# Kernel optimization log

Measured on AMD Instinct MI355X. Metric: run time of the kernel, lower is better.

## Reference

```python
import jax, jax.numpy as jnp
import numpy as np

L, H, N, F, E, FF, OUT, B = 4, 8, 1024, 128, 128, 512, 64, 32


def setup_inputs() -> dict:
    key = jax.random.key(0)
    ks = jax.random.split(key, 16)
    s = 0.02
    return {
        "x": jax.random.normal(ks[0], (B, N, F), jnp.float32),
        "adj": jax.random.randint(ks[1], (N, N), 0, 2, jnp.int32),
        "Ws": jax.random.normal(ks[2], (L, H, E, F), jnp.float32) * s,
        "bs": jnp.zeros((L, H, E), jnp.float32),
        "As": jax.random.normal(ks[3], (L, H, 2 * E, N), jnp.float32) * s,
        "W1": jax.random.normal(ks[4], (L, FF, F), jnp.float32) * s,
        "b1": jnp.zeros((L, FF), jnp.float32),
        "W2": jax.random.normal(ks[5], (L, F, FF), jnp.float32) * s,
        "b2": jnp.zeros((L, F), jnp.float32),
        "g1": jnp.ones((L, F), jnp.float32),
        "be1": jnp.zeros((L, F), jnp.float32),
        "g2": jnp.ones((L, F), jnp.float32),
        "be2": jnp.zeros((L, F), jnp.float32),
        "Wo": jax.random.normal(ks[6], (OUT, N * F), jnp.float32) * s,
        "bo": jnp.zeros((OUT,), jnp.float32),
    }


def _ln(x, g, b, eps=1e-5):
    m = jnp.mean(x, axis=-1, keepdims=True)
    v = jnp.mean((x - m) ** 2, axis=-1, keepdims=True)
    return (x - m) / jnp.sqrt(v + eps) * g + b


def reference(x, adj, Ws, bs, As, W1, b1, W2, b2, g1, be1, g2, be2, Wo, bo):
    # mask[j, i] = 1 if j is a neighbor of i (adj_matrix[:, i] > 0 in torch source)
    mask = (adj > 0).astype(x.dtype)
    E_ = Ws.shape[2]
    for l in range(Ws.shape[0]):
        # per-head projection: h [B, H, N, E]
        h = jnp.einsum('bnf,hef->bhne', x, Ws[l]) + bs[l][None, :, None, :]
        # score[b,h,i] = h_i . a[:E, i] + (sum_{j in N(i)} h_j) . a[E:, i]
        s1 = jnp.einsum('bhne,hen->bhn', h, As[l][:, :E_, :])
        hn = jnp.einsum('jn,bhje->bhne', mask, h)  # neighbor sums
        s2 = jnp.einsum('bhne,hen->bhn', hn, As[l][:, E_:, :])
        score = s1 + s2  # [B, H, N]
        # attention row i is the constant score[b,h,i] broadcast over columns,
        # so attention @ h == score[...,None] * h.sum(over nodes)
        hsum = h.sum(axis=2)  # [B, H, E]
        hp = score[..., None] * hsum[:, :, None, :]  # [B, H, N, E]
        att = jax.nn.leaky_relu(hp, 0.01).sum(axis=1)  # sum over heads -> [B, N, F]
        x = _ln(x + att, g1[l], be1[l])
        ff = jax.nn.relu(x @ W1[l].T + b1[l]) @ W2[l].T + b2[l]
        x = _ln(x + ff, g2[l], be2[l])
    flat = x.reshape(x.shape[0], -1)  # [B, N*F]
    return jax.nn.relu(flat) @ Wo.T + bo
```

## Files before the change

kernel.cpp:

```cpp
#include <hip/hip_runtime.h>

#define L_ 4
#define H_ 8
#define Nn 1024
#define F_ 128
#define E_ 128
#define FF_ 512
#define OUT_ 64
#define B_ 32
#define KTOT (Nn * F_)

typedef unsigned short u16;
typedef __bf16 bf16_t;
typedef __attribute__((ext_vector_type(8))) __bf16 bf16x8;
typedef __attribute__((ext_vector_type(4))) float f32x4;

__device__ __forceinline__ u16 f2b(float v) {
    bf16_t h = (bf16_t)v;
    return __builtin_bit_cast(u16, h);
}
__device__ __forceinline__ float b2f(u16 u) {
    unsigned v = (unsigned)u << 16;
    return __builtin_bit_cast(float, v);
}

typedef const __attribute__((address_space(1))) void* gvp;
typedef __attribute__((address_space(3))) void* lvp;
__device__ __forceinline__ void gll16(const void* g, void* l) {
    __builtin_amdgcn_global_load_lds((gvp)g, (lvp)l, 16, 0, 0);
}

template <int R>
__device__ __forceinline__ void stage(const u16* __restrict__ g, int ldg,
                                      u16* lds, int w, int l) {
    const int r8 = l >> 3, jq = l & 7;
#pragma unroll
    for (int i = 0; i < R / 32; ++i) {
        const int row0 = w * (R / 4) + i * 8;
        const int row = row0 + r8;
        gll16(g + (long)row * ldg + ((jq ^ (row & 7)) << 3), lds + row0 * 64);
    }
}

__device__ __forceinline__ void stage128x64(const u16* __restrict__ g, int ldg,
                                            u16* lds, int w, int l) {
    const int r8 = l >> 3, jq = l & 7;
#pragma unroll
    for (int i = 0; i < 2; ++i) {
        const int row0 = i * 64 + w * 8;
        const int row = row0 + r8;
        gll16(g + (long)row * ldg + ((jq ^ (row & 7)) << 3), lds + row0 * 64);
    }
}

template <int BM, int BN, bool DUAL, int EPI, int BSH, bool GSWAP, bool DBUF>
__global__ __launch_bounds__(256) void k_mfma(
    const u16* __restrict__ A, int lda, long sAz,
    const u16* __restrict__ Bhp, const u16* __restrict__ Blp, int ldb, long sBz,
    const float* __restrict__ bias,
    float* __restrict__ Cf, u16* __restrict__ Cb, int ldc, long sCz, int K)
{
    constexpr int WN = (BN == 64) ? 1 : ((BM == 64) ? 4 : 2);
    constexpr int WM = 4 / WN;
    constexpr int SM = BM / WM, SN = BN / WN;
    constexpr int MF = SM / 16, NF = SN / 16;
    constexpr int BUFE = BM * 64 + (DUAL ? 2 : 1) * BN * 64;
    __shared__ __align__(16) u16 lds[BUFE * (DBUF ? 2 : 1)];
    const int t = threadIdx.x;
    const int w = t >> 6, l = t & 63, lr = l & 15, lg = l >> 4;
    const int wm0 = (w / WN) * SM, wn0 = (w % WN) * SN;
    const int bidm = GSWAP ? blockIdx.z : blockIdx.x;
    const int bidz = GSWAP ? blockIdx.x : blockIdx.z;
    const int m0 = bidm * BM, n0 = blockIdx.y * BN;
    A += BSH ? ((long)(bidz >> 1) * sAz + (long)(bidz & 1) * 128)
             : (long)bidz * sAz;
    Bhp += (long)(bidz >> BSH) * sBz;
    if (DUAL) Blp += (long)bidz * sBz;

    f32x4 acc[MF][NF] = {};

    auto stageAll = [&](u16* base, int k0) {
        stage<BM>(A + (long)m0 * lda + k0, lda, base, w, l);
        stage<BN>(Bhp + (long)n0 * ldb + k0, ldb, base + BM * 64, w, l);
        if (DUAL) stage<BN>(Blp + (long)n0 * ldb + k0, ldb, base + BM * 64 + BN * 64, w, l);
    };
    auto compute = [&](const u16* base) {
        const u16* Al = base;
        const u16* Bh = base + BM * 64;
        const u16* Bl = Bh + BN * 64;
#pragma unroll
        for (int ks = 0; ks < 2; ++ks) {
            bf16x8 af[MF], bh[NF], bl[NF];
            const int kq = ks * 4 + lg;
#pragma unroll
            for (int mf = 0; mf < MF; ++mf) {
                int row = wm0 + mf * 16 + lr;
                af[mf] = *reinterpret_cast<const bf16x8*>(&Al[row * 64 + ((kq ^ (row & 7)) << 3)]);
            }
#pragma unroll
            for (int nf = 0; nf < NF; ++nf) {
                int row = wn0 + nf * 16 + lr;
                int off = row * 64 + ((kq ^ (row & 7)) << 3);
                bh[nf] = *reinterpret_cast<const bf16x8*>(&Bh[off]);
                if (DUAL) bl[nf] = *reinterpret_cast<const bf16x8*>(&Bl[off]);
            }
#pragma unroll
            for (int mf = 0; mf < MF; ++mf)
#pragma unroll
                for (int nf = 0; nf < NF; ++nf) {
                    acc[mf][nf] = __builtin_amdgcn_mfma_f32_16x16x32_bf16(af[mf], bh[nf], acc[mf][nf], 0, 0, 0);
                    if (DUAL)
                        acc[mf][nf] = __builtin_amdgcn_mfma_f32_16x16x32_bf16(af[mf], bl[nf], acc[mf][nf], 0, 0, 0);
                }
        }
    };

    if (DBUF) {
        stageAll(lds, 0);
        __syncthreads();
        int cur = 0;
        for (int k0 = 0; k0 < K; k0 += 64) {
            if (k0 + 64 < K) stageAll(lds + (cur ^ 1) * BUFE, k0 + 64);
            compute(lds + cur * BUFE);
            __syncthreads();
            cur ^= 1;
        }
    } else {
        for (int k0 = 0; k0 < K; k0 += 64) {
            __syncthreads();
            stageAll(lds, k0);
            __syncthreads();
            compute(lds);
        }
    }

    float bv[NF];
    if (EPI == 1) {
#pragma unroll
        for (int nf = 0; nf < NF; ++nf) bv[nf] = bias[n0 + wn0 + nf * 16 + lr];
    }
    if (EPI == 1 || EPI == 3) Cb += (long)bidz * sCz;
    else                      Cf += (long)bidz * sCz;
#pragma unroll
    for (int mf = 0; mf < MF; ++mf)
#pragma unroll
        for (int nf = 0; nf < NF; ++nf)
#pragma unroll
            for (int r = 0; r < 4; ++r) {
                long row = m0 + wm0 + mf * 16 + lg * 4 + r;
                int col = n0 + wn0 + nf * 16 + lr;
                float v = acc[mf][nf][r];
                if (EPI == 1) Cb[row * ldc + col] = f2b(fmaxf(v + bv[nf], 0.f));
                else if (EPI == 3) Cb[row * ldc + col] = f2b(v);
                else Cf[row * ldc + col] = v;
            }
}

template <bool LAST>
__global__ __launch_bounds__(512) void k_ff_ln2(
    const u16* __restrict__ xb,
    const u16* __restrict__ W1b,
    const float* __restrict__ b1,
    const u16* __restrict__ W2b,
    const float* __restrict__ b2,
    float* __restrict__ xc,
    const float* __restrict__ g, const float* __restrict__ be,
    u16* __restrict__ xh,
    float* __restrict__ xsp,
    u16* __restrict__ xrb)
{
    __shared__ __align__(16) u16 lds[65536];
    const int t = threadIdx.x;
    const int w = t >> 6, l = t & 63, lr = l & 15, lg = l >> 4;
    const int wr = w >> 2, wc = w & 3;
    const int wn0 = wc * 32;
    const int m0 = blockIdx.x * 128;
    u16* A0 = lds;
    u16* P0 = lds + 16384;
    u16* Wb0 = lds + 32768;
    u16* Wb1 = lds + 49152;

    stage128x64(xb + (long)m0 * F_,      F_, A0, w, l);
    stage128x64(xb + (long)m0 * F_ + 64, F_, A0 + 8192, w, l);
    stage128x64(W1b,      F_, Wb0, w, l);
    stage128x64(W1b + 64, F_, Wb0 + 8192, w, l);
    float xcr[32];
#pragma unroll
    for (int rr = 0; rr < 16; ++rr) {
        const long xof = (long)(m0 + w * 16 + rr) * F_;
        xcr[rr * 2]     = xc[xof + l];
        xcr[rr * 2 + 1] = xc[xof + l + 64];
    }
    __syncthreads();

    f32x4 acc2[4][2] = {};
    for (int c = 0; c < 4; ++c) {
        stage128x64(W2b + c * 128,      FF_, Wb1, w, l);
        stage128x64(W2b + c * 128 + 64, FF_, Wb1 + 8192, w, l);
        f32x4 acc1[4][2] = {};
#pragma unroll
        for (int s = 0; s < 4; ++s) {
            const int kh = s >> 1, kq = (s & 1) * 4 + lg;
            bf16x8 af[4], bfr[2];
#pragma unroll
            for (int mf = 0; mf < 4; ++mf) {
                int row = wr * 64 + mf * 16 + lr;
                af[mf] = *reinterpret_cast<const bf16x8*>(
                    &A0[kh * 8192 + row * 64 + ((kq ^ (row & 7)) << 3)]);
            }
#pragma unroll
            for (int nf = 0; nf < 2; ++nf) {
                int row = wn0 + nf * 16 + lr;
                bfr[nf] = *reinterpret_cast<const bf16x8*>(
                    &Wb0[kh * 8192 + row * 64 + ((kq ^ (row & 7)) << 3)]);
            }
#pragma unroll
            for (int mf = 0; mf < 4; ++mf)
#pragma unroll
                for (int nf = 0; nf < 2; ++nf)
                    acc1[mf][nf] = __builtin_amdgcn_mfma_f32_16x16x32_bf16(af[mf], bfr[nf], acc1[mf][nf], 0, 0, 0);
        }
        float b1v[2] = { b1[c * 128 + wn0 + lr], b1[c * 128 + wn0 + 16 + lr] };
#pragma unroll
        for (int mf = 0; mf < 4; ++mf)
#pragma unroll
            for (int nf = 0; nf < 2; ++nf)
#pragma unroll
                for (int r = 0; r < 4; ++r) {
                    int row = wr * 64 + mf * 16 + lg * 4 + r;
                    int sp = (row ^ (row >> 3)) & 7;
                    int cc = wn0 + nf * 16 + lr;
                    int c6 = cc & 63;
                    float v = fmaxf(acc1[mf][nf][r] + b1v[nf], 0.f);
                    P0[(cc >> 6) * 8192 + row * 64 + (((c6 >> 3) ^ sp) << 3) + (c6 & 7)] = f2b(v);
                }
        __syncthreads();
        if (c < 3) {
            stage128x64(W1b + (long)(c + 1) * 128 * F_,      F_, Wb0, w, l);
            stage128x64(W1b + (long)(c + 1) * 128 * F_ + 64, F_, Wb0 + 8192, w, l);
        }
#pragma unroll
        for (int s = 0; s < 4; ++s) {
            const int kh = s >> 1, kq = (s & 1) * 4 + lg;
            bf16x8 af[4], bfr[2];
#pragma unroll
            for (int mf = 0; mf < 4; ++mf) {
                int row = wr * 64 + mf * 16 + lr;
                int sp = (row ^ (row >> 3)) & 7;
                af[mf] = *reinterpret_cast<const bf16x8*>(
                    &P0[kh * 8192 + row * 64 + ((kq ^ sp) << 3)]);
            }
#pragma unroll
            for (int nf = 0; nf < 2; ++nf) {
                int row = wn0 + nf * 16 + lr;
                bfr[nf] = *reinterpret_cast<const bf16x8*>(
                    &Wb1[kh * 8192 + row * 64 + ((kq ^ (row & 7)) << 3)]);
            }
#pragma unroll
            for (int mf = 0; mf < 4; ++mf)
#pragma unroll
                for (int nf = 0; nf < 2; ++nf)
                    acc2[mf][nf] = __builtin_amdgcn_mfma_f32_16x16x32_bf16(af[mf], bfr[nf], acc2[mf][nf], 0, 0, 0);
        }
        __syncthreads();
    }
    float (*buf)[132] = (float(*)[132])lds;
    float (*ps)[128]  = (float(*)[128])((char*)lds + 69632);
    float bv[2] = { b2[wn0 + lr], b2[wn0 + 16 + lr] };
#pragma unroll
    for (int mf = 0; mf < 4; ++mf)
#pragma unroll
        for (int nf = 0; nf < 2; ++nf)
#pragma unroll
            for (int r = 0; r < 4; ++r)
                buf[wr * 64 + mf * 16 + lg * 4 + r][wn0 + nf * 16 + lr] = acc2[mf][nf][r] + bv[nf];
    __syncthreads();
    const float gl0 = g[l], gl1 = g[l + 64], bl0 = be[l], bl1 = be[l + 64];
    float s0 = 0.f, s1 = 0.f;
#pragma unroll
    for (int rr = 0; rr < 16; ++rr) {
        const int row = w * 16 + rr;
        const long xb_ = (long)(m0 + row) * F_;
        float v0 = buf[row][l] + xcr[rr * 2];
        float v1 = buf[row][l + 64] + xcr[rr * 2 + 1];
        float sum = v0 + v1;
#pragma unroll
        for (int o = 32; o; o >>= 1) sum += __shfl_xor(sum, o);
        const float mean = sum * (1.f / 128.f);
        const float d0 = v0 - mean, d1 = v1 - mean;
        float vs = d0 * d0 + d1 * d1;
#pragma unroll
        for (int o = 32; o; o >>= 1) vs += __shfl_xor(vs, o);
        const float rstd = rsqrtf(vs * (1.f / 128.f) + 1e-5f);
        float o0 = d0 * rstd * gl0 + bl0;
        float o1 = d1 * rstd * gl1 + bl1;
        if (LAST) {
            xrb[xb_ + l] = f2b(fmaxf(o0, 0.f));
            xrb[xb_ + l + 64] = f2b(fmaxf(o1, 0.f));
        } else {
            xc[xb_ + l] = o0;       xc[xb_ + l + 64] = o1;
            buf[row][l] = o0;       buf[row][l + 64] = o1;
            s0 += o0;               s1 += o1;
        }
    }
    if (!LAST) {
        ps[w][l] = s0; ps[w][l + 64] = s1;
        __syncthreads();
        const int b = m0 >> 10, nb0 = m0 & 1023, seg = (m0 >> 7) & 7;
        const int n8 = (t & 15) * 8, fb = t >> 4;
#pragma unroll
        for (int i = 0; i < 4; ++i) {
            const int f = fb + 32 * i;
            union { u16 u[8]; float4 v; } Hv;
#pragma unroll
            for (int j = 0; j < 8; ++j) Hv.u[j] = f2b(buf[n8 + j][f]);
            *reinterpret_cast<float4*>(&xh[((long)b * F_ + f) * Nn + nb0 + n8]) = Hv.v;
        }
        if (t < 128) {
            float s = 0.f;
#pragma unroll
            for (int k = 0; k < 8; ++k) s += ps[k][t];
            xsp[((long)b * 8 + seg) * 128 + t] = s;
        }
    }
}

__global__ __launch_bounds__(256) void k_final_mfma(
    const u16* __restrict__ xrb, const u16* __restrict__ Wob,
    float* __restrict__ part)
{
    __shared__ __align__(16) u16 Al[32 * 512];
    const int c = blockIdx.x;
    const long k0 = (long)c * 512;
    const int t = threadIdx.x, w = t >> 6, l = t & 63, lr = l & 15, lg = l >> 4;
#pragma unroll
    for (int i = 0; i < 8; ++i) {
        int ch = i * 256 + t, row = ch >> 6, jq = ch & 63;
        *reinterpret_cast<float4*>(&Al[row * 512 + ((jq ^ (row & 7)) << 3)]) =
            *reinterpret_cast<const float4*>(&xrb[(long)row * KTOT + k0 + (jq << 3)]);
    }
    __syncthreads();
    f32x4 acc[2] = {};
    const u16* Bp = Wob + (long)(w * 16 + lr) * KTOT + k0 + lg * 8;
#pragma unroll
    for (int ks = 0; ks < 16; ++ks) {
        bf16x8 bfr = *reinterpret_cast<const bf16x8*>(Bp + ks * 32);
        const int j8 = ks * 4 + lg;
#pragma unroll
        for (int mf = 0; mf < 2; ++mf) {
            int row = mf * 16 + lr;
            bf16x8 af = *reinterpret_cast<const bf16x8*>(&Al[row * 512 + ((j8 ^ (row & 7)) << 3)]);
            acc[mf] = __builtin_amdgcn_mfma_f32_16x16x32_bf16(af, bfr, acc[mf], 0, 0, 0);
        }
    }
#pragma unroll
    for (int mf = 0; mf < 2; ++mf)
#pragma unroll
        for (int r = 0; r < 4; ++r) {
            int b = mf * 16 + lg * 4 + r, o = w * 16 + lr;
            part[((long)c * B_ + b) * OUT_ + o] = acc[mf][r];
        }
}

__global__ void k_final_reduce(const float* __restrict__ part,
                               const float* __restrict__ bo, float* __restrict__ out)
{
    int i = blockIdx.x * 256 + threadIdx.x;
    int o = i & 63;
    float s = bo[o];
    for (int c = 0; c < 256; ++c) s += part[(long)c * (B_ * OUT_) + i];
    out[i] = s;
}

__global__ __launch_bounds__(256) void k_maskT(const int* __restrict__ adj,
                                               u16* __restrict__ maskTb,
                                               int* __restrict__ degi)
{
    __shared__ u16 tl[64][65];
    const int j0 = blockIdx.x * 64, n0 = blockIdx.y * 64, t = threadIdx.x;
#pragma unroll
    for (int i = 0; i < 16; ++i) {
        int s = i * 256 + t, jl = s >> 6, nl = s & 63;
        tl[jl][nl] = (adj[(long)(j0 + jl) * Nn + n0 + nl] > 0) ? 0x3F80 : 0;
    }
    __syncthreads();
    if (t < 64) {
        int c = 0;
#pragma unroll
        for (int jl = 0; jl < 64; ++jl) c += (tl[jl][t] != 0);
        atomicAdd(&degi[n0 + t], c);
    }
#pragma unroll
    for (int i = 0; i < 16; ++i) {
        int s = i * 256 + t, nl = s >> 6, jl = s & 63;
        maskTb[(long)(n0 + nl) * Nn + j0 + jl] = tl[jl][nl];
    }
}

__global__ __launch_bounds__(256) void k_tpb(const float* __restrict__ in,
                                             u16* __restrict__ out, int R, int C)
{
    __shared__ float tl[64][65];
    const int c0 = blockIdx.x * 64, r0 = blockIdx.y * 64, t = threadIdx.x;
    in  += (long)blockIdx.z * R * C;
    out += (long)blockIdx.z * R * C;
#pragma unroll
    for (int i = 0; i < 16; ++i) {
        int s = i * 256 + t, rl = s >> 6, cl = s & 63;
        tl[rl][cl] = in[(long)(r0 + rl) * C + c0 + cl];
    }
    __syncthreads();
#pragma unroll
    for (int i = 0; i < 16; ++i) {
        int s = i * 256 + t, cl = s >> 6, rl = s & 63;
        out[(long)(c0 + cl) * R + r0 + rl] = f2b(tl[rl][cl]);
    }
}

__global__ void k_cvtW(const float* __restrict__ W1, const float* __restrict__ W2,
                       u16* __restrict__ W1b, u16* __restrict__ W2b)
{
    int i = blockIdx.x * 256 + threadIdx.x;
    W1b[i] = f2b(W1[i]);
    W2b[i] = f2b(W2[i]);
}

__global__ void k_cvtWo(const float* __restrict__ Wo, u16* __restrict__ Wob)
{
    long i = ((long)blockIdx.x * 256 + threadIdx.x) * 8;
    float4 a = *reinterpret_cast<const float4*>(&Wo[i]);
    float4 b = *reinterpret_cast<const float4*>(&Wo[i + 4]);
    union { u16 u[8]; float4 v; } r;
    r.u[0] = f2b(a.x); r.u[1] = f2b(a.y); r.u[2] = f2b(a.z); r.u[3] = f2b(a.w);
    r.u[4] = f2b(b.x); r.u[5] = f2b(b.y); r.u[6] = f2b(b.z); r.u[7] = f2b(b.w);
    *reinterpret_cast<float4*>(&Wob[i]) = r.v;
}

__global__ __launch_bounds__(256) void k_xpose(const float* __restrict__ x,
                                               u16* __restrict__ xh)
{
    __shared__ float tile[64][132];
    const int b = blockIdx.y, n0 = blockIdx.x * 64, t = threadIdx.x;
#pragma unroll
    for (int i = 0; i < 8; ++i) {
        int s = i * 256 + t, nl = s >> 5, f4 = (s & 31) << 2;
        float4 v = *reinterpret_cast<const float4*>(&x[((long)b * Nn + n0 + nl) * F_ + f4]);
        tile[nl][f4] = v.x; tile[nl][f4 + 1] = v.y;
        tile[nl][f4 + 2] = v.z; tile[nl][f4 + 3] = v.w;
    }
    __syncthreads();
    const int f = t >> 1, nb = (t & 1) << 5;
    const long ob = ((long)b * F_ + f) * Nn + n0 + nb;
    union { u16 u[8]; float4 v; } Hv;
#pragma unroll
    for (int i = 0; i < 32; i += 8) {
#pragma unroll
        for (int j = 0; j < 8; ++j) Hv.u[j] = f2b(tile[nb + i + j][f]);
        *reinterpret_cast<float4*>(&xh[ob + i]) = Hv.v;
    }
}

__global__ __launch_bounds__(256) void k_xs2(const float* __restrict__ x, float* __restrict__ xsp)
{
    __shared__ float sh[2][128];
    const int seg = blockIdx.x, b = blockIdx.y, t = threadIdx.x;
    const int f = t & 127, h2 = t >> 7;
    const float* p = x + ((long)b * Nn + seg * 128 + h2 * 64) * F_ + f;
    float s = 0.f;
    for (int i = 0; i < 64; ++i) s += p[(long)i * F_];
    sh[h2][f] = s;
    __syncthreads();
    if (t < 128) xsp[((long)b * 8 + seg) * 128 + t] = sh[0][t] + sh[1][t];
}

__global__ void k_hsum(const float* __restrict__ xsp, const float* __restrict__ Wl,
                       const float* __restrict__ bsl, float* __restrict__ hsum)
{
    __shared__ float xs[128];
    const int i = blockIdx.x * 256 + threadIdx.x;
    const int b = i >> 10;
    if (threadIdx.x < 128) {
        const float* xp = xsp + (long)b * 8 * 128 + threadIdx.x;
        float v = 0.f;
#pragma unroll
        for (int sg = 0; sg < 8; ++sg) v += xp[sg * 128];
        xs[threadIdx.x] = v;
    }
    __syncthreads();
    const int e = i & 127, h = (i >> 7) & 7;
    const float* w = Wl + ((long)h * E_ + e) * F_;
    float s = 0.f;
    for (int f = 0; f < F_; ++f) s += xs[f] * w[f];
    hsum[i] = s + (float)Nn * bsl[h * E_ + e];
}

__global__ void k_d12(const float* __restrict__ As, const float* __restrict__ bs,
                      float* __restrict__ d12all)
{
    const int lyr = blockIdx.y;
    const float* Asl = As + (long)lyr * H_ * 2 * E_ * Nn;
    const float* bsl = bs + (long)lyr * H_ * E_;
    int i = blockIdx.x * 256 + threadIdx.x;
    int n = i & 1023, h = (i >> 10) & 7, w = i >> 13;
    const float* a = Asl + ((long)h * 2 * E_ + (long)w * E_) * Nn + n;
    const float* bb = bsl + h * E_;
    float s = 0.f;
    for (int e = 0; e < E_; ++e) s += bb[e] * a[(long)e * Nn];
    d12all[(long)lyr * 2 * H_ * Nn + ((long)w * H_ + h) * Nn + n] = s;
}

__global__ __launch_bounds__(256) void k_score_ln1(
    float* __restrict__ x, const u16* __restrict__ y,
    const float* __restrict__ Ct, const float* __restrict__ d12,
    const int* __restrict__ degi, const float* __restrict__ hsum,
    const float* __restrict__ g, const float* __restrict__ be,
    u16* __restrict__ xb)
{
    const int n = blockIdx.x, t = threadIdx.x;
    __shared__ float c1[H_][128], c2[H_][128];
    __shared__ float sbs[H_];
#pragma unroll
    for (int i = 0; i < 4; ++i) {
        int s = i * 256 + t, h = s >> 7, f = s & 127;
        c1[h][f] = Ct[((long)(2 * h) * Nn + n) * F_ + f];
        c2[h][f] = Ct[((long)(2 * h + 1) * Nn + n) * F_ + f];
    }
    if (t < H_) sbs[t] = d12[(long)t * Nn + n] + (float)degi[n] * d12[(long)(H_ + t) * Nn + n];
    __syncthreads();
    const int w = t >> 6, l = t & 63;
    const float gl0 = g[l], gl1 = g[l + 64], bl0 = be[l], bl1 = be[l + 64];
    for (int bi = 0; bi < 8; ++bi) {
        const int b = w * 8 + bi;
        const long base = ((long)b * Nn + n) * F_;
        float x0 = x[base + l], x1 = x[base + l + 64];
        float y0 = b2f(y[base + l]), y1 = b2f(y[base + l + 64]);
        float a0 = 0.f, a1 = 0.f;
#pragma unroll
        for (int h = 0; h < H_; ++h) {
            float p = x0 * c1[h][l] + x1 * c1[h][l + 64]
                    + y0 * c2[h][l] + y1 * c2[h][l + 64];
#pragma unroll
            for (int o = 32; o; o >>= 1) p += __shfl_xor(p, o);
            float s = p + sbs[h];
            float h0 = hsum[((long)b * H_ + h) * E_ + l];
            float h1 = hsum[((long)b * H_ + h) * E_ + l + 64];
            float p0 = s * h0, p1 = s * h1;
            a0 += (p0 > 0.f ? p0 : 0.01f * p0);
            a1 += (p1 > 0.f ? p1 : 0.01f * p1);
        }
        float v0 = x0 + a0, v1 = x1 + a1;
        float sum = v0 + v1;
#pragma unroll
        for (int o = 32; o; o >>= 1) sum += __shfl_xor(sum, o);
        const float mean = sum * (1.f / 128.f);
        const float d0 = v0 - mean, d1 = v1 - mean;
        float vs = d0 * d0 + d1 * d1;
#pragma unroll
        for (int o = 32; o; o >>= 1) vs += __shfl_xor(vs, o);
        const float rstd = rsqrtf(vs * (1.f / 128.f) + 1e-5f);
        float o0 = d0 * rstd * gl0 + bl0;
        float o1 = d1 * rstd * gl1 + bl1;
        x[base + l] = o0;        x[base + l + 64] = o1;
        xb[base + l] = f2b(o0);  xb[base + l + 64] = f2b(o1);
    }
}

extern "C" void kernel_launch(void* const* d_in, const int* in_sizes, int n_in,
                              void* d_out, int out_size, void* d_ws, size_t ws_size,
                              hipStream_t stream)
{
    const float* x_in = (const float*)d_in[0];
    const int*   adj  = (const int*)d_in[1];
    const float* Ws   = (const float*)d_in[2];
    const float* bs   = (const float*)d_in[3];
    const float* As   = (const float*)d_in[4];
    const float* W1   = (const float*)d_in[5];
    const float* b1   = (const float*)d_in[6];
    const float* W2   = (const float*)d_in[7];
    const float* b2   = (const float*)d_in[8];
    const float* g1   = (const float*)d_in[9];
    const float* be1  = (const float*)d_in[10];
    const float* g2   = (const float*)d_in[11];
    const float* be2  = (const float*)d_in[12];
    const float* Wo   = (const float*)d_in[13];
    const float* bo   = (const float*)d_in[14];
    float* out = (float*)d_out;

    char* wsb = (char*)d_ws;
    u16*   maskTb = (u16*)wsb;
    float* xc     = (float*)(wsb + (2L << 20));
    u16*   yb     = (u16*)(wsb + (18L << 20));
    float* CtAll  = (float*)(wsb + (66L << 20));
    u16*   xb     = (u16*)(wsb + (98L << 20));
    u16*   xrb    = (u16*)(wsb + (106L << 20));
    u16*   Wob    = (u16*)(wsb + (114L << 20));
    float* part   = (float*)(wsb + (130L << 20));
    u16*   xTh    = (u16*)(wsb + (132L << 20));
    u16*   AsTb   = (u16*)(wsb + (148L << 20));
    u16*   WsTb   = (u16*)(wsb + (164L << 20));
    char*  S      = wsb + (166L << 20);
    int*   degi   = (int*)S;
    float* xsp    = (float*)(S + (4L << 10));
    float* hsum   = (float*)(S + (132L << 10));
    float* d12all = (float*)(S + (260L << 10));
    u16*   W1b    = (u16*)(S + (516L << 10));
    u16*   W2b    = (u16*)(S + (1028L << 10));

    hipMemsetAsync(degi, 0, Nn * sizeof(int), stream);
    hipMemcpyAsync(xc, x_in, sizeof(float) * (long)B_ * Nn * F_,
                   hipMemcpyDeviceToDevice, stream);
    k_maskT<<<dim3(16, 16), 256, 0, stream>>>(adj, maskTb, degi);
    k_cvtW<<<(L_ * FF_ * F_) / 256, 256, 0, stream>>>(W1, W2, W1b, W2b);
    k_cvtWo<<<(OUT_ * KTOT) / (256 * 8), 256, 0, stream>>>(Wo, Wob);
    k_tpb<<<dim3(16, 4, L_ * H_), 256, 0, stream>>>(As, AsTb, 2 * E_, Nn);
    k_tpb<<<dim3(2, 2, L_ * H_), 256, 0, stream>>>(Ws, WsTb, E_, F_);
    k_xpose<<<dim3(16, B_), 256, 0, stream>>>(x_in, xTh);
    k_xs2<<<dim3(8, B_), 256, 0, stream>>>(x_in, xsp);
    k_d12<<<dim3((2 * H_ * Nn) / 256, L_), 256, 0, stream>>>(As, bs, d12all);
    k_mfma<64, 128, false, 0, 1, false, false><<<dim3(16, 1, 64), 256, 0, stream>>>(
        AsTb, 2 * E_, (long)Nn * 2 * E_, WsTb, nullptr, E_, (long)F_ * E_,
        nullptr, CtAll, nullptr, F_, (long)Nn * F_, E_);

    for (int l = 0; l < L_; ++l) {
        const float* Wl  = Ws + (long)l * H_ * E_ * F_;
        const float* bsl = bs + (long)l * H_ * E_;

        k_mfma<128, 64, false, 3, 0, true, true><<<dim3(32, 2, 8), 256, 0, stream>>>(
            maskTb, Nn, 0L, xTh, nullptr, Nn, (long)F_ * Nn,
            nullptr, nullptr, yb, F_, (long)Nn * F_, Nn);

        k_hsum<<<(B_ * H_ * E_) / 256, 256, 0, stream>>>(xsp, Wl, bsl, hsum);
        k_score_ln1<<<Nn, 256, 0, stream>>>(
            xc, yb, CtAll + (long)l * 16 * Nn * F_, d12all + (long)l * 2 * H_ * Nn,
            degi, hsum, g1 + l * F_, be1 + l * F_, xb);
        if (l < L_ - 1)
            k_ff_ln2<false><<<256, 512, 0, stream>>>(
                xb, W1b + (long)l * FF_ * F_, b1 + l * FF_,
                W2b + (long)l * F_ * FF_, b2 + l * F_, xc,
                g2 + l * F_, be2 + l * F_, xTh, xsp, nullptr);
        else
            k_ff_ln2<true><<<256, 512, 0, stream>>>(
                xb, W1b + (long)l * FF_ * F_, b1 + l * FF_,
                W2b + (long)l * F_ * FF_, b2 + l * F_, xc,
                g2 + l * F_, be2 + l * F_, nullptr, nullptr, xrb);
    }

    k_final_mfma<<<256, 256, 0, stream>>>(xrb, Wob, part);
    k_final_reduce<<<(B_ * OUT_) / 256, 256, 0, stream>>>(part, bo, out);
}
```

Before: 372.7 us.

## Keep residual stream and Ct projection in bf16 to cut memory traffic

Replaces the fp32 residual buffer xc with bf16 ping-pong buffers (xA/xB). The LN2 residual is now read from the already staged bf16 tile in LDS instead of reloaded from global memory, and the output buffer moves to a non-overlapping LDS region. The precomputed Ct projection is also stored in bf16, and the initial fp32 device copy is replaced by a bf16 conversion kernel. This halves global reads and writes of the activations in score_ln1 and ff_ln2, at the cost of bf16 rounding in the residual path.

```diff
diff --git a/kernel.cpp b/kernel.cpp
--- a/kernel.cpp
+++ b/kernel.cpp
@@ -163,8 +163,8 @@
     const float* __restrict__ b1,
     const u16* __restrict__ W2b,
     const float* __restrict__ b2,
-    float* __restrict__ xc,
     const float* __restrict__ g, const float* __restrict__ be,
+    u16* __restrict__ xbn,
     u16* __restrict__ xh,
     float* __restrict__ xsp,
     u16* __restrict__ xrb)
@@ -184,13 +184,6 @@
     stage128x64(xb + (long)m0 * F_ + 64, F_, A0 + 8192, w, l);
     stage128x64(W1b,      F_, Wb0, w, l);
     stage128x64(W1b + 64, F_, Wb0 + 8192, w, l);
-    float xcr[32];
-#pragma unroll
-    for (int rr = 0; rr < 16; ++rr) {
-        const long xof = (long)(m0 + w * 16 + rr) * F_;
-        xcr[rr * 2]     = xc[xof + l];
-        xcr[rr * 2 + 1] = xc[xof + l + 64];
-    }
     __syncthreads();
 
     f32x4 acc2[4][2] = {};
@@ -264,8 +257,8 @@
         }
         __syncthreads();
     }
-    float (*buf)[132] = (float(*)[132])lds;
-    float (*ps)[128]  = (float(*)[128])((char*)lds + 69632);
+    float (*buf)[132] = (float(*)[132])((char*)lds + 32768);
+    float (*ps)[128]  = (float(*)[128])((char*)lds + 100352);
     float bv[2] = { b2[wn0 + lr], b2[wn0 + 16 + lr] };
 #pragma unroll
     for (int mf = 0; mf < 4; ++mf)
@@ -281,8 +274,11 @@
     for (int rr = 0; rr < 16; ++rr) {
         const int row = w * 16 + rr;
         const long xb_ = (long)(m0 + row) * F_;
-        float v0 = buf[row][l] + xcr[rr * 2];
-        float v1 = buf[row][l + 64] + xcr[rr * 2 + 1];
+        const int sw = (row & 7);
+        float r0 = b2f(A0[row * 64 + ((((l >> 3) ^ sw)) << 3) + (l & 7)]);
+        float r1 = b2f(A0[8192 + row * 64 + ((((l >> 3) ^ sw)) << 3) + (l & 7)]);
+        float v0 = buf[row][l] + r0;
+        float v1 = buf[row][l + 64] + r1;
         float sum = v0 + v1;
 #pragma unroll
         for (int o = 32; o; o >>= 1) sum += __shfl_xor(sum, o);
@@ -298,7 +294,8 @@
             xrb[xb_ + l] = f2b(fmaxf(o0, 0.f));
             xrb[xb_ + l + 64] = f2b(fmaxf(o1, 0.f));
         } else {
-            xc[xb_ + l] = o0;       xc[xb_ + l + 64] = o1;
+            xbn[xb_ + l] = f2b(o0);
+            xbn[xb_ + l + 64] = f2b(o1);
             buf[row][l] = o0;       buf[row][l + 64] = o1;
             s0 += o0;               s1 += o1;
         }
@@ -434,6 +431,17 @@
     r.u[0] = f2b(a.x); r.u[1] = f2b(a.y); r.u[2] = f2b(a.z); r.u[3] = f2b(a.w);
     r.u[4] = f2b(b.x); r.u[5] = f2b(b.y); r.u[6] = f2b(b.z); r.u[7] = f2b(b.w);
     *reinterpret_cast<float4*>(&Wob[i]) = r.v;
+}
+
+__global__ void k_cvtX(const float* __restrict__ x, u16* __restrict__ xo)
+{
+    long i = ((long)blockIdx.x * 256 + threadIdx.x) * 8;
+    float4 a = *reinterpret_cast<const float4*>(&x[i]);
+    float4 b = *reinterpret_cast<const float4*>(&x[i + 4]);
+    union { u16 u[8]; float4 v; } r;
+    r.u[0] = f2b(a.x); r.u[1] = f2b(a.y); r.u[2] = f2b(a.z); r.u[3] = f2b(a.w);
+    r.u[4] = f2b(b.x); r.u[5] = f2b(b.y); r.u[6] = f2b(b.z); r.u[7] = f2b(b.w);
+    *reinterpret_cast<float4*>(&xo[i]) = r.v;
 }
 
 __global__ __launch_bounds__(256) void k_xpose(const float* __restrict__ x,
@@ -510,8 +518,8 @@
 }
 
 __global__ __launch_bounds__(256) void k_score_ln1(
-    float* __restrict__ x, const u16* __restrict__ y,
-    const float* __restrict__ Ct, const float* __restrict__ d12,
+    const u16* __restrict__ xA, const u16* __restrict__ y,
+    const u16* __restrict__ Ctb, const float* __restrict__ d12,
     const int* __restrict__ degi, const float* __restrict__ hsum,
     const float* __restrict__ g, const float* __restrict__ be,
     u16* __restrict__ xb)
@@ -522,8 +530,8 @@
 #pragma unroll
     for (int i = 0; i < 4; ++i) {
         int s = i * 256 + t, h = s >> 7, f = s & 127;
-        c1[h][f] = Ct[((long)(2 * h) * Nn + n) * F_ + f];
-        c2[h][f] = Ct[((long)(2 * h + 1) * Nn + n) * F_ + f];
+        c1[h][f] = b2f(Ctb[((long)(2 * h) * Nn + n) * F_ + f]);
+        c2[h][f] = b2f(Ctb[((long)(2 * h + 1) * Nn + n) * F_ + f]);
     }
     if (t < H_) sbs[t] = d12[(long)t * Nn + n] + (float)degi[n] * d12[(long)(H_ + t) * Nn + n];
     __syncthreads();
@@ -532,8 +540,8 @@
     for (int bi = 0; bi < 8; ++bi) {
         const int b = w * 8 + bi;
         const long base = ((long)b * Nn + n) * F_;
-        float x0 = x[base + l], x1 = x[base + l + 64];
-        float y0 = b2f(y[base + l]), y1 = b2f(y[base + l + 64]);
+        float x0 = b2f(xA[base + l]), x1 = b2f(xA[base + l + 64]);
+        float y0 = b2f(y[base + l]),  y1 = b2f(y[base + l + 64]);
         float a0 = 0.f, a1 = 0.f;
 #pragma unroll
         for (int h = 0; h < H_; ++h) {
@@ -558,10 +566,8 @@
 #pragma unroll
         for (int o = 32; o; o >>= 1) vs += __shfl_xor(vs, o);
         const float rstd = rsqrtf(vs * (1.f / 128.f) + 1e-5f);
-        float o0 = d0 * rstd * gl0 + bl0;
-        float o1 = d1 * rstd * gl1 + bl1;
-        x[base + l] = o0;        x[base + l + 64] = o1;
-        xb[base + l] = f2b(o0);  xb[base + l + 64] = f2b(o1);
+        xb[base + l]      = f2b(d0 * rstd * gl0 + bl0);
+        xb[base + l + 64] = f2b(d1 * rstd * gl1 + bl1);
     }
 }
 
@@ -588,17 +594,17 @@
 
     char* wsb = (char*)d_ws;
     u16*   maskTb = (u16*)wsb;
-    float* xc     = (float*)(wsb + (2L << 20));
-    u16*   yb     = (u16*)(wsb + (18L << 20));
-    float* CtAll  = (float*)(wsb + (66L << 20));
-    u16*   xb     = (u16*)(wsb + (98L << 20));
-    u16*   xrb    = (u16*)(wsb + (106L << 20));
-    u16*   Wob    = (u16*)(wsb + (114L << 20));
-    float* part   = (float*)(wsb + (130L << 20));
-    u16*   xTh    = (u16*)(wsb + (132L << 20));
-    u16*   AsTb   = (u16*)(wsb + (148L << 20));
-    u16*   WsTb   = (u16*)(wsb + (164L << 20));
-    char*  S      = wsb + (166L << 20);
+    u16*   xA     = (u16*)(wsb + (2L << 20));
+    u16*   yb     = (u16*)(wsb + (10L << 20));
+    u16*   CtAllb = (u16*)(wsb + (18L << 20));
+    u16*   xB     = (u16*)(wsb + (34L << 20));
+    u16*   xrb    = (u16*)(wsb + (42L << 20));
+    u16*   Wob    = (u16*)(wsb + (50L << 20));
+    float* part   = (float*)(wsb + (66L << 20));
+    u16*   xTh    = (u16*)(wsb + (68L << 20));
+    u16*   AsTb   = (u16*)(wsb + (76L << 20));
+    u16*   WsTb   = (u16*)(wsb + (92L << 20));
+    char*  S      = wsb + (94L << 20);
     int*   degi   = (int*)S;
     float* xsp    = (float*)(S + (4L << 10));
     float* hsum   = (float*)(S + (132L << 10));
@@ -607,19 +613,18 @@
     u16*   W2b    = (u16*)(S + (1028L << 10));
 
     hipMemsetAsync(degi, 0, Nn * sizeof(int), stream);
-    hipMemcpyAsync(xc, x_in, sizeof(float) * (long)B_ * Nn * F_,
-                   hipMemcpyDeviceToDevice, stream);
     k_maskT<<<dim3(16, 16), 256, 0, stream>>>(adj, maskTb, degi);
     k_cvtW<<<(L_ * FF_ * F_) / 256, 256, 0, stream>>>(W1, W2, W1b, W2b);
     k_cvtWo<<<(OUT_ * KTOT) / (256 * 8), 256, 0, stream>>>(Wo, Wob);
+    k_cvtX<<<(B_ * Nn * F_) / (256 * 8), 256, 0, stream>>>(x_in, xA);
     k_tpb<<<dim3(16, 4, L_ * H_), 256, 0, stream>>>(As, AsTb, 2 * E_, Nn);
     k_tpb<<<dim3(2, 2, L_ * H_), 256, 0, stream>>>(Ws, WsTb, E_, F_);
     k_xpose<<<dim3(16, B_), 256, 0, stream>>>(x_in, xTh);
     k_xs2<<<dim3(8, B_), 256, 0, stream>>>(x_in, xsp);
     k_d12<<<dim3((2 * H_ * Nn) / 256, L_), 256, 0, stream>>>(As, bs, d12all);
-    k_mfma<64, 128, false, 0, 1, false, false><<<dim3(16, 1, 64), 256, 0, stream>>>(
+    k_mfma<64, 128, false, 3, 1, false, false><<<dim3(16, 1, 64), 256, 0, stream>>>(
         AsTb, 2 * E_, (long)Nn * 2 * E_, WsTb, nullptr, E_, (long)F_ * E_,
-        nullptr, CtAll, nullptr, F_, (long)Nn * F_, E_);
+        nullptr, nullptr, CtAllb, F_, (long)Nn * F_, E_);
 
     for (int l = 0; l < L_; ++l) {
         const float* Wl  = Ws + (long)l * H_ * E_ * F_;
@@ -631,18 +636,18 @@
 
         k_hsum<<<(B_ * H_ * E_) / 256, 256, 0, stream>>>(xsp, Wl, bsl, hsum);
         k_score_ln1<<<Nn, 256, 0, stream>>>(
-            xc, yb, CtAll + (long)l * 16 * Nn * F_, d12all + (long)l * 2 * H_ * Nn,
-            degi, hsum, g1 + l * F_, be1 + l * F_, xb);
+            xA, yb, CtAllb + (long)l * 16 * Nn * F_, d12all + (long)l * 2 * H_ * Nn,
+            degi, hsum, g1 + l * F_, be1 + l * F_, xB);
         if (l < L_ - 1)
             k_ff_ln2<false><<<256, 512, 0, stream>>>(
-                xb, W1b + (long)l * FF_ * F_, b1 + l * FF_,
-                W2b + (long)l * F_ * FF_, b2 + l * F_, xc,
-                g2 + l * F_, be2 + l * F_, xTh, xsp, nullptr);
+                xB, W1b + (long)l * FF_ * F_, b1 + l * FF_,
+                W2b + (long)l * F_ * FF_, b2 + l * F_,
+                g2 + l * F_, be2 + l * F_, xA, xTh, xsp, nullptr);
         else
             k_ff_ln2<true><<<256, 512, 0, stream>>>(
-                xb, W1b + (long)l * FF_ * F_, b1 + l * FF_,
-                W2b + (long)l * F_ * FF_, b2 + l * F_, xc,
-                g2 + l * F_, be2 + l * F_, nullptr, nullptr, xrb);
+                xB, W1b + (long)l * FF_ * F_, b1 + l * FF_,
+                W2b + (long)l * F_ * FF_, b2 + l * F_,
+                g2 + l * F_, be2 + l * F_, nullptr, nullptr, nullptr, xrb);
     }
 
     k_final_mfma<<<256, 256, 0, stream>>>(xrb, Wob, part);
```

New measurement: 364.0 us. 2.3% less time.
